# Optimization experiments

Hardware: AMD Instinct MI355X
Metric: run time of the kernel (lower is better)

The kernel has to match this reference:

```python
import jax, jax.numpy as jnp
import numpy as np

N_NODES = 50000
N_EDGES = 800000
F_IN = 256
HID = 64
HEADS = 4
NEG_SLOPE = 0.2


def setup_inputs() -> dict:
    key = jax.random.key(0)
    ks = jax.random.split(key, 12)
    x = jax.random.normal(ks[0], (N_NODES, F_IN), dtype=jnp.float32)
    src = jax.random.randint(ks[1], (N_EDGES,), 0, N_NODES)
    dst = jax.random.randint(ks[2], (N_EDGES,), 0, N_NODES)
    s0 = 1.0 / np.sqrt(F_IN)
    s1 = 1.0 / np.sqrt(HEADS * HID)
    W0 = jax.random.normal(ks[3], (F_IN, HEADS * HID), dtype=jnp.float32) * s0
    a_l0 = jax.random.normal(ks[4], (HEADS, HID), dtype=jnp.float32) * s1
    a_r0 = jax.random.normal(ks[5], (HEADS, HID), dtype=jnp.float32) * s1
    b0 = jnp.zeros((HEADS * HID,), dtype=jnp.float32)
    W1 = jax.random.normal(ks[6], (HEADS * HID, HEADS * HID), dtype=jnp.float32) * s1
    a_l1 = jax.random.normal(ks[7], (HEADS, HID), dtype=jnp.float32) * s1
    a_r1 = jax.random.normal(ks[8], (HEADS, HID), dtype=jnp.float32) * s1
    b1 = jnp.zeros((HEADS * HID,), dtype=jnp.float32)
    return {"x": x, "src": src, "dst": dst,
            "W0": W0, "a_l0": a_l0, "a_r0": a_r0, "b0": b0,
            "W1": W1, "a_l1": a_l1, "a_r1": a_r1, "b1": b1}


def _gat_layer(h, src, dst, W, a_l, a_r, b):
    # h: [N, F_in] -> feat: [N, H, D]
    feat = (h @ W).reshape(h.shape[0], HEADS, HID)
    el = jnp.sum(feat * a_l, axis=-1)  # [N, H]
    er = jnp.sum(feat * a_r, axis=-1)  # [N, H]
    e = jax.nn.leaky_relu(el[src] + er[dst], NEG_SLOPE)  # [E, H]
    # per-destination edge softmax (numerically stable)
    m = jax.ops.segment_max(e, dst, num_segments=N_NODES)  # [N, H]
    ex = jnp.exp(e - m[dst])
    s = jax.ops.segment_sum(ex, dst, num_segments=N_NODES)  # [N, H]
    alpha = ex / jnp.maximum(s[dst], 1e-9)  # [E, H]
    msg = feat[src] * alpha[:, :, None]  # [E, H, D]
    rst = jax.ops.segment_sum(msg, dst, num_segments=N_NODES)  # [N, H, D]
    rst = rst + b.reshape(1, HEADS, HID)
    return jax.nn.elu(rst)


def reference(x, src, dst, W0, a_l0, a_r0, b0, W1, a_l1, a_r1, b1):
    h = _gat_layer(x, src, dst, W0, a_l0, a_r0, b0)  # [N, H, D]
    h = h.reshape(N_NODES, HEADS * HID)              # flatten(1)
    h = _gat_layer(h, src, dst, W1, a_l1, a_r1, b1)  # [N, H, D]
    # list of per-head outputs h[:, i]
    return tuple(h[:, i] for i in range(HEADS))
```

## Files before the change

kernel.cpp:

```cpp
#include <hip/hip_runtime.h>
#include <math.h>

#define N_NODES 50000
#define N_EDGES 800000
#define HEADS 4
#define HID 64
#define FDIM 256
#define LDA 40
#define SCAN_CHUNK 1024
#define SCAN_NB ((N_NODES + SCAN_CHUNK - 1) / SCAN_CHUNK)

typedef __attribute__((ext_vector_type(8))) _Float16 half8;
typedef __attribute__((ext_vector_type(4))) _Float16 half4;
typedef __attribute__((ext_vector_type(4))) float f32x4;


__global__ __launch_bounds__(256) void hist_kernel(const int* __restrict__ dst,
                                                   int* __restrict__ counts, int E) {
    int i = blockIdx.x * blockDim.x + threadIdx.x;
    if (i < E) atomicAdd(&counts[dst[i]], 1);
}

__global__ __launch_bounds__(256) void scan_local(const int* __restrict__ counts,
                                                  int* __restrict__ offs,
                                                  int* __restrict__ bsum, int n) {
    __shared__ int part[256];
    const int b = blockIdx.x, t = threadIdx.x;
    const int base = b * SCAN_CHUNK + t * 4;
    int v[4];
#pragma unroll
    for (int j = 0; j < 4; j++) {
        int idx = base + j;
        v[j] = (idx < n) ? counts[idx] : 0;
    }
    int s0 = v[0], s1 = s0 + v[1], s2 = s1 + v[2], s3 = s2 + v[3];
    part[t] = s3;
    __syncthreads();
    for (int off = 1; off < 256; off <<= 1) {
        int x = (t >= off) ? part[t - off] : 0;
        __syncthreads();
        part[t] += x;
        __syncthreads();
    }
    int prefix = (t > 0) ? part[t - 1] : 0;
    int e[4] = {prefix, prefix + s0, prefix + s1, prefix + s2};
#pragma unroll
    for (int j = 0; j < 4; j++) {
        int idx = base + j;
        if (idx < n) offs[idx] = e[j];
    }
    if (t == 255) bsum[b] = part[255];
}

__global__ __launch_bounds__(64) void scan_bsum(int* __restrict__ bsum,
                                                int* __restrict__ offs, int nb, int n) {
    int lane = threadIdx.x;
    int own = (lane < nb) ? bsum[lane] : 0;
    int v = own;
    for (int off = 1; off < 64; off <<= 1) {
        int x = __shfl_up(v, off);
        if (lane >= off) v += x;
    }
    if (lane < nb) bsum[lane] = v - own;
    if (lane == nb - 1) offs[n] = v;
}

__global__ __launch_bounds__(256) void scan_add(int* __restrict__ offs,
                                                const int* __restrict__ bsum, int n) {
    const int b = blockIdx.x;
    const int p = bsum[b];
    const int base = b * SCAN_CHUNK + threadIdx.x * 4;
#pragma unroll
    for (int j = 0; j < 4; j++) {
        int idx = base + j;
        if (idx < n) offs[idx] += p;
    }
}

__global__ __launch_bounds__(256) void scatter_kernel(const int* __restrict__ src,
                                                      const int* __restrict__ dst,
                                                      const int* __restrict__ offs,
                                                      int* __restrict__ cursor,
                                                      int* __restrict__ csr_src, int E) {
    int i = blockIdx.x * blockDim.x + threadIdx.x;
    if (i < E) {
        int d = dst[i];
        int p = offs[d] + atomicAdd(&cursor[d], 1);
        csr_src[p] = src[i];
    }
}


__global__ __launch_bounds__(256) void wcast_kernel(const float* __restrict__ W0,
                                                    const float* __restrict__ W1,
                                                    _Float16* __restrict__ wt0,
                                                    _Float16* __restrict__ wt1) {
    const float* W = blockIdx.y ? W1 : W0;
    _Float16* wt = blockIdx.y ? wt1 : wt0;
    int n = blockIdx.x * 16 + (threadIdx.x >> 4);
    int k0 = (threadIdx.x & 15) * 16;
    for (int j = 0; j < 16; j++)
        wt[n * FDIM + k0 + j] = (_Float16)W[(k0 + j) * FDIM + n];
}

__global__ __launch_bounds__(256) void cast_x_kernel(const float* __restrict__ x,
                                                     _Float16* __restrict__ x16) {
    size_t i = ((size_t)blockIdx.x * 256 + threadIdx.x) * 4;
    float4 v = *(const float4*)&x[i];
    half4 h = {(_Float16)v.x, (_Float16)v.y, (_Float16)v.z, (_Float16)v.w};
    *(half4*)&x16[i] = h;
}

__global__ __launch_bounds__(256) void mfma_gemm(const _Float16* __restrict__ A16,
                                                 const _Float16* __restrict__ Bt,
                                                 const float* __restrict__ al,
                                                 const float* __restrict__ ar,
                                                 _Float16* __restrict__ feat16,
                                                 float* __restrict__ el,
                                                 float* __restrict__ er) {
    __shared__ _Float16 ash[128][LDA];
    __shared__ _Float16 bsh[128][LDA];

    const int t = threadIdx.x;
    const int m0 = blockIdx.x * 128;
    const int n0 = blockIdx.y * 128;
    const int wave = t >> 6, lane = t & 63;
    const int quad = lane >> 4, l16 = lane & 15;
    const int wr = (wave >> 1) * 64;
    const int wc = (wave & 1) * 64;

    const f32x4 zero = {0.f, 0.f, 0.f, 0.f};
    f32x4 acc[4][4];
#pragma unroll
    for (int i = 0; i < 4; i++)
#pragma unroll
        for (int j = 0; j < 4; j++) acc[i][j] = zero;

    for (int kk = 0; kk < FDIM; kk += 32) {
#pragma unroll
        for (int ii = 0; ii < 2; ii++) {
            int idx = t + ii * 256;
            int row = idx >> 2;
            int kb = (idx & 3) * 8;
            int gr = m0 + row; if (gr >= N_NODES) gr = N_NODES - 1;
            *(half8*)&ash[row][kb] = *(const half8*)&A16[(size_t)gr * FDIM + kk + kb];
            *(half8*)&bsh[row][kb] = *(const half8*)&Bt[(size_t)(n0 + row) * FDIM + kk + kb];
        }
        __syncthreads();

        half8 af[4], bf[4];
#pragma unroll
        for (int i = 0; i < 4; i++) {
            af[i] = *(half8*)&ash[wr + i * 16 + l16][quad * 8];
            bf[i] = *(half8*)&bsh[wc + i * 16 + l16][quad * 8];
        }
#pragma unroll
        for (int mt = 0; mt < 4; mt++)
#pragma unroll
            for (int nt = 0; nt < 4; nt++)
                acc[mt][nt] = __builtin_amdgcn_mfma_f32_16x16x32_f16(af[mt], bf[nt], acc[mt][nt], 0, 0, 0);
        __syncthreads();
    }

    const int h = (n0 + wc) >> 6;
    float alv[4], arv[4];
#pragma unroll
    for (int nt = 0; nt < 4; nt++) {
        alv[nt] = al[n0 + wc + nt * 16 + l16];
        arv[nt] = ar[n0 + wc + nt * 16 + l16];
    }
#pragma unroll
    for (int mt = 0; mt < 4; mt++) {
        int m = m0 + wr + mt * 16 + quad * 4;
        float pl[4] = {0.f, 0.f, 0.f, 0.f}, pr[4] = {0.f, 0.f, 0.f, 0.f};
#pragma unroll
        for (int nt = 0; nt < 4; nt++) {
            int n = n0 + wc + nt * 16 + l16;
#pragma unroll
            for (int r = 0; r < 4; r++) {
                float v = acc[mt][nt][r];
                if (m + r < N_NODES) feat16[(size_t)(m + r) * FDIM + n] = (_Float16)v;
                pl[r] += v * alv[nt];
                pr[r] += v * arv[nt];
            }
        }
#pragma unroll
        for (int r = 0; r < 4; r++) {
            float a = pl[r], b = pr[r];
            for (int off = 8; off; off >>= 1) {
                a += __shfl_down(a, off, 16);
                b += __shfl_down(b, off, 16);
            }
            if (l16 == 0 && m + r < N_NODES) {
                el[(m + r) * 4 + h] = a;
                er[(m + r) * 4 + h] = b;
            }
        }
    }
}

__global__ __launch_bounds__(256) void agg_fused(const _Float16* __restrict__ feat16,
                                                 const float* __restrict__ el,
                                                 const float* __restrict__ er,
                                                 const float* __restrict__ bias,
                                                 const int* __restrict__ offs,
                                                 const int* __restrict__ csr_src,
                                                 float* __restrict__ out,
                                                 _Float16* __restrict__ h1,
                                                 int mode) {
    const int wave = threadIdx.x >> 6;
    const int lane = threadIdx.x & 63;
    const int n = blockIdx.x * 4 + wave;
    const int head = lane >> 4;
    const int f = lane * 4;
    const int base16 = lane & 48;
    const int j16 = lane & 15;
    const int beg = offs[n];
    const int end = offs[n + 1];
    const float er_h = er[n * 4 + head];

    float4 acc = make_float4(0.f, 0.f, 0.f, 0.f);
    float ss = 0.f;

    for (int c = beg; c < end; c += 16) {
        int e = c + j16;
        int s_own = 0;
        float w_own = 0.f;
        if (e < end) {
            s_own = csr_src[e];
            float lg = el[s_own * 4 + head] + er_h;
            lg = (lg > 0.f) ? lg : 0.2f * lg;
            w_own = __expf(lg);
        }
        ss += w_own;

        int rem = end - c;
        if (rem > 16) rem = 16;

        int j = 0;
        for (; j + 3 < rem; j += 4) {
            int s0 = __shfl(s_own, base16 + j);
            int s1 = __shfl(s_own, base16 + j + 1);
            int s2 = __shfl(s_own, base16 + j + 2);
            int s3 = __shfl(s_own, base16 + j + 3);
            float w0 = __shfl(w_own, base16 + j);
            float w1 = __shfl(w_own, base16 + j + 1);
            float w2 = __shfl(w_own, base16 + j + 2);
            float w3 = __shfl(w_own, base16 + j + 3);
            half4 v0 = *(const half4*)&feat16[(size_t)s0 * FDIM + f];
            half4 v1 = *(const half4*)&feat16[(size_t)s1 * FDIM + f];
            half4 v2 = *(const half4*)&feat16[(size_t)s2 * FDIM + f];
            half4 v3 = *(const half4*)&feat16[(size_t)s3 * FDIM + f];
            acc.x += w0 * (float)v0[0] + w1 * (float)v1[0];
            acc.y += w0 * (float)v0[1] + w1 * (float)v1[1];
            acc.z += w0 * (float)v0[2] + w1 * (float)v1[2];
            acc.w += w0 * (float)v0[3] + w1 * (float)v1[3];
            acc.x += w2 * (float)v2[0] + w3 * (float)v3[0];
            acc.y += w2 * (float)v2[1] + w3 * (float)v3[1];
            acc.z += w2 * (float)v2[2] + w3 * (float)v3[2];
            acc.w += w2 * (float)v2[3] + w3 * (float)v3[3];
        }
        for (; j < rem; j++) {
            int s0 = __shfl(s_own, base16 + j);
            float w0 = __shfl(w_own, base16 + j);
            half4 v0 = *(const half4*)&feat16[(size_t)s0 * FDIM + f];
            acc.x += w0 * (float)v0[0];
            acc.y += w0 * (float)v0[1];
            acc.z += w0 * (float)v0[2];
            acc.w += w0 * (float)v0[3];
        }
    }

    ss += __shfl_xor(ss, 1, 16);
    ss += __shfl_xor(ss, 2, 16);
    ss += __shfl_xor(ss, 4, 16);
    ss += __shfl_xor(ss, 8, 16);

    float S = fmaxf(ss, 1e-9f);
    float inv = 1.f / S;
    float4 bv = *(const float4*)&bias[f];
    float r0 = acc.x * inv + bv.x;
    float r1 = acc.y * inv + bv.y;
    float r2 = acc.z * inv + bv.z;
    float r3 = acc.w * inv + bv.w;
    r0 = (r0 > 0.f) ? r0 : expm1f(r0);
    r1 = (r1 > 0.f) ? r1 : expm1f(r1);
    r2 = (r2 > 0.f) ? r2 : expm1f(r2);
    r3 = (r3 > 0.f) ? r3 : expm1f(r3);

    if (mode) {
        const int d = (lane & 15) * 4;
        float4 rv = make_float4(r0, r1, r2, r3);
        *(float4*)&out[(size_t)head * N_NODES * HID + (size_t)n * HID + d] = rv;
    } else {
        half4 hv = {(_Float16)r0, (_Float16)r1, (_Float16)r2, (_Float16)r3};
        *(half4*)&h1[(size_t)n * FDIM + f] = hv;
    }
}


extern "C" void kernel_launch(void* const* d_in, const int* in_sizes, int n_in,
                              void* d_out, int out_size, void* d_ws, size_t ws_size,
                              hipStream_t stream) {
    const float* x   = (const float*)d_in[0];
    const int*   src = (const int*)d_in[1];
    const int*   dst = (const int*)d_in[2];
    const float* W0  = (const float*)d_in[3];
    const float* al0 = (const float*)d_in[4];
    const float* ar0 = (const float*)d_in[5];
    const float* b0  = (const float*)d_in[6];
    const float* W1  = (const float*)d_in[7];
    const float* al1 = (const float*)d_in[8];
    const float* ar1 = (const float*)d_in[9];
    const float* b1  = (const float*)d_in[10];
    float* out = (float*)d_out;

    _Float16* x16h1 = (_Float16*)d_out;

    _Float16* feat16 = (_Float16*)d_ws;
    _Float16* wt0 = feat16 + (size_t)N_NODES * FDIM;
    _Float16* wt1 = wt0 + FDIM * FDIM;
    float* el    = (float*)(wt1 + FDIM * FDIM);
    float* er    = el + N_NODES * HEADS;
    int* counts  = (int*)(er + N_NODES * HEADS);
    int* cursor  = counts + N_NODES;
    int* offs    = cursor + N_NODES;
    int* bsum    = offs + 50016;
    int* csr_src = bsum + 64;

    hipMemsetAsync(counts, 0, 2 * N_NODES * sizeof(int), stream);
    wcast_kernel<<<dim3(16, 2), 256, 0, stream>>>(W0, W1, wt0, wt1);
    cast_x_kernel<<<N_NODES * FDIM / 1024, 256, 0, stream>>>(x, x16h1);
    hist_kernel<<<(N_EDGES + 255) / 256, 256, 0, stream>>>(dst, counts, N_EDGES);
    scan_local<<<SCAN_NB, 256, 0, stream>>>(counts, offs, bsum, N_NODES);
    scan_bsum<<<1, 64, 0, stream>>>(bsum, offs, SCAN_NB, N_NODES);
    scan_add<<<SCAN_NB, 256, 0, stream>>>(offs, bsum, N_NODES);
    scatter_kernel<<<(N_EDGES + 255) / 256, 256, 0, stream>>>(src, dst, offs, cursor, csr_src, N_EDGES);

    dim3 ggrid((N_NODES + 127) / 128, FDIM / 128);

    mfma_gemm<<<ggrid, 256, 0, stream>>>(x16h1, wt0, al0, ar0, feat16, el, er);
    agg_fused<<<N_NODES / 4, 256, 0, stream>>>(feat16, el, er, b0, offs, csr_src,
                                               out, x16h1, 0);

    mfma_gemm<<<ggrid, 256, 0, stream>>>(x16h1, wt1, al1, ar1, feat16, el, er);
    agg_fused<<<N_NODES / 4, 256, 0, stream>>>(feat16, el, er, b1, offs, csr_src,
                                               out, x16h1, 1);
}
```

Before: 390.2 us.

## Fuse x fp32-to-fp16 cast into GEMM and widen tile to full N

Removes the separate cast_x kernel: the layer-0 GEMM now reads fp32 x directly and converts it to fp16 while staging into shared memory. The GEMM block grows to 512 threads and covers all 256 output columns, so each A row tile is loaded once instead of twice across two column blocks. This saves a full write-and-read pass of the fp16 copy of x and halves A traffic. In exchange the grid is half as large, with more LDS and registers per block, which may lower occupancy.

```diff
diff --git a/kernel.cpp b/kernel.cpp
--- a/kernel.cpp
+++ b/kernel.cpp
@@ -103,15 +103,9 @@
         wt[n * FDIM + k0 + j] = (_Float16)W[(k0 + j) * FDIM + n];
 }
 
-__global__ __launch_bounds__(256) void cast_x_kernel(const float* __restrict__ x,
-                                                     _Float16* __restrict__ x16) {
-    size_t i = ((size_t)blockIdx.x * 256 + threadIdx.x) * 4;
-    float4 v = *(const float4*)&x[i];
-    half4 h = {(_Float16)v.x, (_Float16)v.y, (_Float16)v.z, (_Float16)v.w};
-    *(half4*)&x16[i] = h;
-}
-
-__global__ __launch_bounds__(256) void mfma_gemm(const _Float16* __restrict__ A16,
+template <int A32>
+__global__ __launch_bounds__(512) void mfma_gemm(const _Float16* __restrict__ A16,
+                                                 const float* __restrict__ Af,
                                                  const _Float16* __restrict__ Bt,
                                                  const float* __restrict__ al,
                                                  const float* __restrict__ ar,
@@ -119,15 +113,14 @@
                                                  float* __restrict__ el,
                                                  float* __restrict__ er) {
     __shared__ _Float16 ash[128][LDA];
-    __shared__ _Float16 bsh[128][LDA];
+    __shared__ _Float16 bsh[256][LDA];
 
     const int t = threadIdx.x;
     const int m0 = blockIdx.x * 128;
-    const int n0 = blockIdx.y * 128;
     const int wave = t >> 6, lane = t & 63;
     const int quad = lane >> 4, l16 = lane & 15;
-    const int wr = (wave >> 1) * 64;
-    const int wc = (wave & 1) * 64;
+    const int wr = (wave >> 2) * 64;
+    const int wc = (wave & 3) * 64;
 
     const f32x4 zero = {0.f, 0.f, 0.f, 0.f};
     f32x4 acc[4][4];
@@ -137,14 +130,27 @@
         for (int j = 0; j < 4; j++) acc[i][j] = zero;
 
     for (int kk = 0; kk < FDIM; kk += 32) {
+        {
+            int row = t >> 2;
+            int kb = (t & 3) * 8;
+            int gr = m0 + row; if (gr >= N_NODES) gr = N_NODES - 1;
+            if (A32) {
+                const float* p = &Af[(size_t)gr * FDIM + kk + kb];
+                float4 f0 = *(const float4*)p;
+                float4 f1 = *(const float4*)(p + 4);
+                half8 hv = {(_Float16)f0.x, (_Float16)f0.y, (_Float16)f0.z, (_Float16)f0.w,
+                            (_Float16)f1.x, (_Float16)f1.y, (_Float16)f1.z, (_Float16)f1.w};
+                *(half8*)&ash[row][kb] = hv;
+            } else {
+                *(half8*)&ash[row][kb] = *(const half8*)&A16[(size_t)gr * FDIM + kk + kb];
+            }
+        }
 #pragma unroll
         for (int ii = 0; ii < 2; ii++) {
-            int idx = t + ii * 256;
+            int idx = t + ii * 512;
             int row = idx >> 2;
             int kb = (idx & 3) * 8;
-            int gr = m0 + row; if (gr >= N_NODES) gr = N_NODES - 1;
-            *(half8*)&ash[row][kb] = *(const half8*)&A16[(size_t)gr * FDIM + kk + kb];
-            *(half8*)&bsh[row][kb] = *(const half8*)&Bt[(size_t)(n0 + row) * FDIM + kk + kb];
+            *(half8*)&bsh[row][kb] = *(const half8*)&Bt[(size_t)row * FDIM + kk + kb];
         }
         __syncthreads();
 
@@ -162,12 +168,12 @@
         __syncthreads();
     }
 
-    const int h = (n0 + wc) >> 6;
+    const int h = wc >> 6;
     float alv[4], arv[4];
 #pragma unroll
     for (int nt = 0; nt < 4; nt++) {
-        alv[nt] = al[n0 + wc + nt * 16 + l16];
-        arv[nt] = ar[n0 + wc + nt * 16 + l16];
+        alv[nt] = al[wc + nt * 16 + l16];
+        arv[nt] = ar[wc + nt * 16 + l16];
     }
 #pragma unroll
     for (int mt = 0; mt < 4; mt++) {
@@ -175,7 +181,7 @@
         float pl[4] = {0.f, 0.f, 0.f, 0.f}, pr[4] = {0.f, 0.f, 0.f, 0.f};
 #pragma unroll
         for (int nt = 0; nt < 4; nt++) {
-            int n = n0 + wc + nt * 16 + l16;
+            int n = wc + nt * 16 + l16;
 #pragma unroll
             for (int r = 0; r < 4; r++) {
                 float v = acc[mt][nt][r];
@@ -315,7 +321,7 @@
     const float* b1  = (const float*)d_in[10];
     float* out = (float*)d_out;
 
-    _Float16* x16h1 = (_Float16*)d_out;
+    _Float16* h1 = (_Float16*)d_out;
 
     _Float16* feat16 = (_Float16*)d_ws;
     _Float16* wt0 = feat16 + (size_t)N_NODES * FDIM;
@@ -330,20 +336,19 @@
 
     hipMemsetAsync(counts, 0, 2 * N_NODES * sizeof(int), stream);
     wcast_kernel<<<dim3(16, 2), 256, 0, stream>>>(W0, W1, wt0, wt1);
-    cast_x_kernel<<<N_NODES * FDIM / 1024, 256, 0, stream>>>(x, x16h1);
     hist_kernel<<<(N_EDGES + 255) / 256, 256, 0, stream>>>(dst, counts, N_EDGES);
     scan_local<<<SCAN_NB, 256, 0, stream>>>(counts, offs, bsum, N_NODES);
     scan_bsum<<<1, 64, 0, stream>>>(bsum, offs, SCAN_NB, N_NODES);
     scan_add<<<SCAN_NB, 256, 0, stream>>>(offs, bsum, N_NODES);
     scatter_kernel<<<(N_EDGES + 255) / 256, 256, 0, stream>>>(src, dst, offs, cursor, csr_src, N_EDGES);
 
-    dim3 ggrid((N_NODES + 127) / 128, FDIM / 128);
-
-    mfma_gemm<<<ggrid, 256, 0, stream>>>(x16h1, wt0, al0, ar0, feat16, el, er);
+    const int ggrid = (N_NODES + 127) / 128;
+
+    mfma_gemm<1><<<ggrid, 512, 0, stream>>>(nullptr, x, wt0, al0, ar0, feat16, el, er);
     agg_fused<<<N_NODES / 4, 256, 0, stream>>>(feat16, el, er, b0, offs, csr_src,
-                                               out, x16h1, 0);
-
-    mfma_gemm<<<ggrid, 256, 0, stream>>>(x16h1, wt1, al1, ar1, feat16, el, er);
+                                               out, h1, 0);
+
+    mfma_gemm<0><<<ggrid, 512, 0, stream>>>(h1, nullptr, wt1, al1, ar1, feat16, el, er);
     agg_fused<<<N_NODES / 4, 256, 0, stream>>>(feat16, el, er, b1, offs, csr_src,
-                                               out, x16h1, 1);
-}
+                                               out, h1, 1);
+}
```

After: 378.9 us. -2.9%, faster.
